# Optimization experiments

Hardware: AMD Instinct MI355X
Metric: run time of the kernel (lower is better)

The kernel has to match this reference:

```python
import jax, jax.numpy as jnp
import numpy as np

DECAY = 0.99
EPS = 1e-5
K = 1024  # num_embeddings
D = 64    # embedding_dim


def setup_inputs() -> dict:
    key = jax.random.key(0)
    k1, k2 = jax.random.split(key)
    inputs = jax.random.normal(k1, (64, 64, 32, 32), dtype=jnp.float32)
    weight = jax.random.uniform(k2, (K, D), minval=-1.0 / K, maxval=1.0 / K, dtype=jnp.float32)
    cluster_size = jnp.zeros((K,), dtype=jnp.float32)
    embed_avg = weight.copy()
    return {"inputs": inputs, "weight": weight, "cluster_size": cluster_size, "embed_avg": embed_avg}


def reference(inputs, weight, cluster_size, embed_avg):
    B, _, H, W = inputs.shape
    # faithful to torch: raw memory-order view(-1, D), no channel permute
    flat = inputs.reshape(-1, D)  # (N, D), N = B*H*W
    distances = (jnp.sum(flat * flat, axis=1, keepdims=True)
                 + jnp.sum(weight * weight, axis=1)
                 - 2.0 * flat @ weight.T)
    idx = jnp.argmin(distances, axis=1)  # (N,)
    quantized = weight[idx].reshape(inputs.shape)  # == onehot @ weight, reshaped

    # EMA codebook update (training path)
    counts = jax.ops.segment_sum(jnp.ones(flat.shape[0], dtype=jnp.float32), idx, num_segments=K)
    cs = DECAY * cluster_size + (1.0 - DECAY) * counts
    n = jnp.sum(cs)
    cs = (cs + EPS) / (n + K * EPS) * n
    dw = jax.ops.segment_sum(flat, idx, num_segments=K)  # == onehot^T @ flat
    new_embed_avg = DECAY * embed_avg + (1.0 - DECAY) * dw
    new_weight = new_embed_avg / cs[:, None]

    # straight-through estimator
    quantized_st = inputs + jax.lax.stop_gradient(quantized - inputs)
    indices = idx.reshape(B, H, W)
    return quantized_st, indices, new_weight, cs, new_embed_avg
```

## Files before the change

kernel.cpp:

```cpp
#include <hip/hip_runtime.h>

#define NROWS 65536
#define KC    1024
#define DD    64

#define QOFF  0
#define IOFF  4194304
#define WOFF  4259840
#define CSOFF 4325376
#define EAOFF 4326400

#define WS_CODESQ  0
#define WS_COUNTS  1056
#define WS_RCCNT   2080
#define WS_CURSOR  2096
#define WS_OFFS    3120
#define WS_CSFIN   4144
#define WS_DW      5168
#define WS_WSWZ    70704
#define WS_IDX     137264
#define WS_RCLIST  202800
#define WS_ROWLIST 268336
#define WS_PACKED  333872

#define MARGIN 5e-5f
#define DECIDED_BIT 0x10000

typedef _Float16 half8 __attribute__((ext_vector_type(8)));
typedef float    floatx4 __attribute__((ext_vector_type(4)));

struct F4 { float x, y, z, w; };
typedef const __attribute__((address_space(4))) F4    c4F4;
typedef const __attribute__((address_space(4))) float c4f;

__device__ __forceinline__ unsigned f2ord(float f) {
    unsigned u = __float_as_uint(f);
    return (u & 0x80000000u) ? ~u : (u | 0x80000000u);
}

__device__ __forceinline__ float med3f(float a, float b, float c) {
    float d;
    asm("v_med3_f32 %0, %1, %2, %3" : "=v"(d) : "v"(a), "v"(b), "v"(c));
    return d;
}

__device__ __forceinline__ float rowsq4(const float4* xv) {
    float4 re, ro;
    re.x = __fmul_rn(xv[0].x, xv[0].x); re.y = __fmul_rn(xv[0].y, xv[0].y);
    re.z = __fmul_rn(xv[0].z, xv[0].z); re.w = __fmul_rn(xv[0].w, xv[0].w);
    ro.x = __fmul_rn(xv[1].x, xv[1].x); ro.y = __fmul_rn(xv[1].y, xv[1].y);
    ro.z = __fmul_rn(xv[1].z, xv[1].z); ro.w = __fmul_rn(xv[1].w, xv[1].w);
#pragma unroll
    for (int i = 2; i < 16; i += 2) {
        re.x = __fadd_rn(re.x, __fmul_rn(xv[i].x, xv[i].x));
        re.y = __fadd_rn(re.y, __fmul_rn(xv[i].y, xv[i].y));
        re.z = __fadd_rn(re.z, __fmul_rn(xv[i].z, xv[i].z));
        re.w = __fadd_rn(re.w, __fmul_rn(xv[i].w, xv[i].w));
        ro.x = __fadd_rn(ro.x, __fmul_rn(xv[i + 1].x, xv[i + 1].x));
        ro.y = __fadd_rn(ro.y, __fmul_rn(xv[i + 1].y, xv[i + 1].y));
        ro.z = __fadd_rn(ro.z, __fmul_rn(xv[i + 1].z, xv[i + 1].z));
        ro.w = __fadd_rn(ro.w, __fmul_rn(xv[i + 1].w, xv[i + 1].w));
    }
    return __fadd_rn(__fadd_rn(__fadd_rn(re.x, re.y), __fadd_rn(re.z, re.w)),
                     __fadd_rn(__fadd_rn(ro.x, ro.y), __fadd_rn(ro.z, ro.w)));
}

__global__ void prep_kernel(const float* __restrict__ weight,
                            float* __restrict__ code_sq,
                            _Float16* __restrict__ wswz,
                            float* __restrict__ counts,
                            int* __restrict__ rccnt) {
    int c = blockIdx.x * blockDim.x + threadIdx.x;
    if (c >= KC) return;
    counts[c] = 0.0f;
    if (c == 0) rccnt[0] = 0;
    float4 wv4[16];
    const float4* pw = reinterpret_cast<const float4*>(weight + (size_t)c * DD);
#pragma unroll
    for (int i = 0; i < 16; ++i) wv4[i] = pw[i];
    code_sq[c] = rowsq4(wv4);
    float w64[64];
#pragma unroll
    for (int i = 0; i < 16; ++i) {
        w64[4 * i] = wv4[i].x; w64[4 * i + 1] = wv4[i].y;
        w64[4 * i + 2] = wv4[i].z; w64[4 * i + 3] = wv4[i].w;
    }
    const int t32 = c >> 5;
    const int s16 = (c >> 4) & 1;
    const int cl  = c & 15;
    const size_t base = (size_t)t32 * 4096 + s16 * 2048 + cl * 8;
#pragma unroll
    for (int q = 0; q < 8; ++q) {
        half8 h, l;
#pragma unroll
        for (int j = 0; j < 8; ++j) {
            float s = w64[q * 8 + j] * 1024.0f;
            _Float16 hh = (_Float16)s;
            h[j] = hh;
            l[j] = (_Float16)(s - (float)hh);
        }
        *reinterpret_cast<half8*>(wswz + base + q * 128)        = h;
        *reinterpret_cast<half8*>(wswz + base + 1024 + q * 128) = l;
    }
}

__global__ __launch_bounds__(256, 4) void vq_scan(
    const float* __restrict__ x_in, const float* __restrict__ weight,
    const float* __restrict__ code_sq, const _Float16* __restrict__ wswz,
    float* __restrict__ out, float* __restrict__ counts,
    int* __restrict__ idxbuf, int* __restrict__ rccnt, int* __restrict__ rclist,
    unsigned long long* __restrict__ packed) {

    __shared__ __align__(16) _Float16 lds_b[2][8192];
    __shared__ float lds_csq[KC];
    __shared__ float sm1[4][32], sm2[4][32];
    __shared__ int   si1[4][32];
    __shared__ int   idx_l[64];

    const int tid  = threadIdx.x;
    const int lane = tid & 63;
    const int w    = tid >> 6;
    const int wm   = w & 1;
    const int wsel = w >> 1;
    const int l15  = lane & 15;
    const int g    = lane >> 4;

    const int blockRow0 = blockIdx.x * 64;
    const int waveRow0  = blockRow0 + wm * 32;

    char* gsrc0 = const_cast<char*>(reinterpret_cast<const char*>(wswz));

#pragma unroll
    for (int j = 0; j < 4; ++j) {
        __builtin_amdgcn_global_load_lds(
            (__attribute__((address_space(1))) void*)(gsrc0 + tid * 16 + j * 4096),
            (__attribute__((address_space(3))) void*)((char*)lds_b[0] + tid * 16 + j * 4096),
            16, 0, 0);
    }

#pragma unroll
    for (int i = 0; i < 4; ++i) lds_csq[tid + i * 256] = code_sq[tid + i * 256];

    half8 ah[4], al[4];
#pragma unroll
    for (int t = 0; t < 2; ++t) {
#pragma unroll
        for (int kh = 0; kh < 2; ++kh) {
            const float4* p4 = reinterpret_cast<const float4*>(
                x_in + (size_t)(waveRow0 + t * 16 + l15) * DD + kh * 32 + g * 8);
            float4 v0 = p4[0], v1 = p4[1];
            float vals[8] = {v0.x, v0.y, v0.z, v0.w, v1.x, v1.y, v1.z, v1.w};
            half8 hh, ll;
#pragma unroll
            for (int j = 0; j < 8; ++j) {
                _Float16 h = (_Float16)vals[j];
                hh[j] = h;
                ll[j] = (_Float16)(vals[j] - (float)h);
            }
            ah[t * 2 + kh] = hh;
            al[t * 2 + kh] = ll;
        }
    }
    __syncthreads();

    float m1[2][4], m2[2][4];
    int   i1[2][4];
#pragma unroll
    for (int t = 0; t < 2; ++t)
#pragma unroll
        for (int r = 0; r < 4; ++r) { m1[t][r] = INFINITY; m2[t][r] = INFINITY; i1[t][r] = 0; }

    int cur = 0;
    for (int p = 0; p < 16; ++p) {
        if (p < 15) {
            char* src = gsrc0 + (size_t)(p + 1) * 16384;
            char* dst = (char*)lds_b[cur ^ 1];
#pragma unroll
            for (int j = 0; j < 4; ++j) {
                __builtin_amdgcn_global_load_lds(
                    (__attribute__((address_space(1))) void*)(src + tid * 16 + j * 4096),
                    (__attribute__((address_space(3))) void*)(dst + tid * 16 + j * 4096),
                    16, 0, 0);
            }
        }

#pragma unroll
        for (int half = 0; half < 2; ++half) {
            const _Float16* S = lds_b[cur] + half * 4096 + wsel * 2048;
            half8 bh0 = *reinterpret_cast<const half8*>(S + g * 128 + l15 * 8);
            half8 bh1 = *reinterpret_cast<const half8*>(S + 512 + g * 128 + l15 * 8);
            half8 bl0 = *reinterpret_cast<const half8*>(S + 1024 + g * 128 + l15 * 8);
            half8 bl1 = *reinterpret_cast<const half8*>(S + 1536 + g * 128 + l15 * 8);
            const int code = p * 64 + half * 32 + wsel * 16 + l15;
            const float csq = lds_csq[code];
#pragma unroll
            for (int t = 0; t < 2; ++t) {
                floatx4 c1 = {0.f, 0.f, 0.f, 0.f};
                floatx4 c2 = {0.f, 0.f, 0.f, 0.f};
                c1 = __builtin_amdgcn_mfma_f32_16x16x32_f16(al[t * 2 + 0], bh0, c1, 0, 0, 0);
                c2 = __builtin_amdgcn_mfma_f32_16x16x32_f16(al[t * 2 + 1], bh1, c2, 0, 0, 0);
                c1 = __builtin_amdgcn_mfma_f32_16x16x32_f16(ah[t * 2 + 0], bl0, c1, 0, 0, 0);
                c2 = __builtin_amdgcn_mfma_f32_16x16x32_f16(ah[t * 2 + 1], bl1, c2, 0, 0, 0);
                c1 = __builtin_amdgcn_mfma_f32_16x16x32_f16(ah[t * 2 + 0], bh0, c1, 0, 0, 0);
                c2 = __builtin_amdgcn_mfma_f32_16x16x32_f16(ah[t * 2 + 1], bh1, c2, 0, 0, 0);
#pragma unroll
                for (int r = 0; r < 4; ++r) {
                    float s = fmaf(c1[r] + c2[r], -0x1p-9f, csq);
                    float mo = m1[t][r];
                    m2[t][r] = med3f(s, mo, m2[t][r]);
                    i1[t][r] = (s < mo) ? code : i1[t][r];
                    m1[t][r] = fminf(mo, s);
                }
            }
        }

        __syncthreads();
        cur ^= 1;
    }

#pragma unroll
    for (int t = 0; t < 2; ++t)
#pragma unroll
        for (int r = 0; r < 4; ++r)
#pragma unroll
            for (int mk = 1; mk < 16; mk <<= 1) {
                float o1 = __shfl_xor(m1[t][r], mk);
                float o2 = __shfl_xor(m2[t][r], mk);
                int   oi = __shfl_xor(i1[t][r], mk);
                float n2 = fminf(fminf(m2[t][r], o2), fmaxf(m1[t][r], o1));
                bool sel = (o1 < m1[t][r]) || (o1 == m1[t][r] && oi < i1[t][r]);
                m1[t][r] = sel ? o1 : m1[t][r];
                i1[t][r] = sel ? oi : i1[t][r];
                m2[t][r] = n2;
            }

    if (l15 == 0) {
#pragma unroll
        for (int t = 0; t < 2; ++t)
#pragma unroll
            for (int r = 0; r < 4; ++r) {
                int rib = t * 16 + g * 4 + r;
                sm1[w][rib] = m1[t][r];
                sm2[w][rib] = m2[t][r];
                si1[w][rib] = i1[t][r];
            }
    }
    __syncthreads();

    if (tid < 64) {
        int pwm = tid >> 5;
        int rib = tid & 31;
        float bm1 = sm1[pwm][rib], bm2 = sm2[pwm][rib];
        int bi = si1[pwm][rib];
        {
            float v1 = sm1[pwm + 2][rib];
            float v2 = sm2[pwm + 2][rib];
            int   vi = si1[pwm + 2][rib];
            if (v1 < bm1 || (v1 == bm1 && vi < bi)) {
                bm2 = fminf(bm1, v2);
                bm1 = v1; bi = vi;
            } else {
                bm2 = fminf(bm2, v1);
            }
        }
        int grow = blockRow0 + tid;
        if (bm2 - bm1 >= MARGIN) {
            idxbuf[grow] = bi | DECIDED_BIT;
            out[IOFF + grow] = (float)bi;
            atomicAdd(&counts[bi], 1.0f);
            idx_l[tid] = bi;
        } else {
            packed[grow] = 0xFFFFFFFFFFFFFFFFull;
            int pos = atomicAdd(rccnt, 1);
            rclist[pos] = grow;
            idx_l[tid] = -1;
        }
    }
    __syncthreads();

    {
        const float4* xin4 = reinterpret_cast<const float4*>(x_in);
        const float4* w4g  = reinterpret_cast<const float4*>(weight);
        float4* q4 = reinterpret_cast<float4*>(out + QOFF);
        const size_t blk4 = (size_t)blockRow0 * 16;
#pragma unroll
        for (int j = 0; j < 4; ++j) {
            int f4i = tid + j * 256;
            int rl  = f4i >> 4;
            int d4  = f4i & 15;
            int idx = idx_l[rl];
            if (idx < 0) continue;
            float4 xq = xin4[blk4 + f4i];
            float4 wq = w4g[idx * 16 + d4];
            float4 qv;
            qv.x = __fadd_rn(xq.x, __fsub_rn(wq.x, xq.x));
            qv.y = __fadd_rn(xq.y, __fsub_rn(wq.y, xq.y));
            qv.z = __fadd_rn(xq.z, __fsub_rn(wq.z, xq.z));
            qv.w = __fadd_rn(xq.w, __fsub_rn(wq.w, xq.w));
            q4[blk4 + f4i] = qv;
        }
    }
}

__global__ __launch_bounds__(256, 4) void vq_recheck(
    const float* __restrict__ x_in, const float* __restrict__ weight,
    const float* __restrict__ code_sq,
    unsigned long long* __restrict__ packed,
    const int* __restrict__ rccnt, const int* __restrict__ rclist) {

    const int nrc = rccnt[0];
    const int nitems = ((nrc + 63) >> 6) * 16;

    const int tid  = threadIdx.x;
    const int lane = tid & 63;
    const int wvu  = __builtin_amdgcn_readfirstlane(tid >> 6);

    for (int item = blockIdx.x; item < nitems; item += gridDim.x) {
        const int rb     = (item >> 4) * 64;
        const int cchunk = item & 15;
        const bool valid = (rb + lane) < nrc;
        const int  grow  = rclist[valid ? rb + lane : rb];

        float4 xv[16];
        const float4* px = reinterpret_cast<const float4*>(x_in + (size_t)grow * DD);
#pragma unroll
        for (int i = 0; i < 16; ++i) xv[i] = px[i];
        const float rs = rowsq4(xv);

        const int k0 = cchunk * 64 + wvu * 16;
        unsigned long long wa = (unsigned long long)(weight + (size_t)k0 * DD);
        unsigned long long ca = (unsigned long long)(code_sq + k0);
        unsigned wal = __builtin_amdgcn_readfirstlane((unsigned)wa);
        unsigned wah = __builtin_amdgcn_readfirstlane((unsigned)(wa >> 32));
        unsigned cal = __builtin_amdgcn_readfirstlane((unsigned)ca);
        unsigned cah = __builtin_amdgcn_readfirstlane((unsigned)(ca >> 32));
        c4F4* wb4 = (c4F4*)(((unsigned long long)wah << 32) | wal);
        c4f*  cb  = (c4f*)(((unsigned long long)cah << 32) | cal);

        float best = INFINITY;
        int bidx = 0x7fffffff;

#pragma unroll 2
        for (int k = 0; k < 16; ++k) {
            float a0 = 0.f, a1 = 0.f, a2 = 0.f, a3 = 0.f;
#pragma unroll
            for (int i = 0; i < 16; ++i) {
                F4 w4;
                w4.x = wb4[k * 16 + i].x;
                w4.y = wb4[k * 16 + i].y;
                w4.z = wb4[k * 16 + i].z;
                w4.w = wb4[k * 16 + i].w;
                a0 += xv[i].x * w4.x;
                a1 += xv[i].y * w4.y;
                a2 += xv[i].z * w4.z;
                a3 += xv[i].w * w4.w;
            }
            float dot = (a0 + a1) + (a2 + a3);
            float csq = cb[k];
            float dst = __fsub_rn(__fadd_rn(rs, csq), __fmul_rn(2.0f, dot));
            int kg = k0 + k;
            if (dst < best) { best = dst; bidx = kg; }
        }

        if (valid) {
            unsigned long long p =
                ((unsigned long long)f2ord(best) << 32) | (unsigned)bidx;
            atomicMin(&packed[grow], p);
        }
    }
}

__global__ void rc_offsets_cs(const unsigned long long* __restrict__ packed,
                              const int* __restrict__ rccnt,
                              const int* __restrict__ rclist,
                              const float* __restrict__ cluster_size,
                              float* __restrict__ out, int* __restrict__ idxbuf,
                              float* __restrict__ counts,
                              int* __restrict__ offs, int* __restrict__ cursor,
                              float* __restrict__ cs_fin) {
    __shared__ int   hist[1024];
    __shared__ int   sc[1024];
    __shared__ float sb[1024];
    int k = threadIdx.x;
    hist[k] = 0;
    __syncthreads();
    const int nrc = rccnt[0];
    for (int i = k; i < nrc; i += 1024) {
        int grow = rclist[i];
        int bidx = (int)(packed[grow] & 0xFFFFFFFFull);
        out[IOFF + grow] = (float)bidx;
        idxbuf[grow] = bidx;
        atomicAdd(&hist[bidx], 1);
    }
    __syncthreads();
    int c = (int)counts[k] + hist[k];
    counts[k] = (float)c;
    float ce = 0.99f * cluster_size[k] + 0.01f * (float)c;
    sc[k] = c;
    sb[k] = ce;
    __syncthreads();
    for (int off = 1; off < 1024; off <<= 1) {
        int v = (k >= off) ? sc[k - off] : 0;
        __syncthreads();
        sc[k] += v;
        __syncthreads();
    }
    offs[k] = sc[k] - c;
    cursor[k] = 0;
    for (int off = 512; off > 0; off >>= 1) {
        if (k < off) sb[k] += sb[k + off];
        __syncthreads();
    }
    float n = sb[0];
    float v = ((ce + 1e-5f) / (n + 0.01024f)) * n;
    out[CSOFF + k] = v;
    cs_fin[k] = v;
}

__global__ void scatter_kernel(const int* __restrict__ idxbuf,
                               const int* __restrict__ offs,
                               int* __restrict__ cursor,
                               int* __restrict__ rowlist) {
    int r = blockIdx.x * blockDim.x + threadIdx.x;
    if (r >= NROWS) return;
    int v = idxbuf[r];
    int k = v & 1023;
    int pos = atomicAdd(&cursor[k], 1);
    rowlist[offs[k] + pos] = r | ((v & DECIDED_BIT) ? 0 : 0x80000000);
}

__global__ __launch_bounds__(512) void dw_q_kernel(
    const float* __restrict__ x_in,
    const float* __restrict__ weight,
    const float* __restrict__ counts,
    const int* __restrict__ offs,
    const int* __restrict__ rowlist,
    const float* __restrict__ embed_avg,
    const float* __restrict__ cs_fin,
    float* __restrict__ out, float* __restrict__ dw) {
    __shared__ float wsh[64];
    __shared__ float part[8][64];

    const int k    = blockIdx.x;
    const int tid  = threadIdx.x;
    const int lane = tid & 63;
    const int wv   = tid >> 6;

    if (tid < 64) wsh[tid] = weight[(size_t)k * DD + tid];
    __syncthreads();

    const int cnt  = (int)counts[k];
    const int base = offs[k];
    const float wk = wsh[lane];

    float acc = 0.f;
    int i = wv;
    for (; i + 24 < cnt; i += 32) {
        int e0 = rowlist[base + i];
        int e1 = rowlist[base + i + 8];
        int e2 = rowlist[base + i + 16];
        int e3 = rowlist[base + i + 24];
        int r0 = e0 & 0x7fffffff;
        int r1 = e1 & 0x7fffffff;
        int r2 = e2 & 0x7fffffff;
        int r3 = e3 & 0x7fffffff;
        float x0 = x_in[(size_t)r0 * DD + lane];
        float x1 = x_in[(size_t)r1 * DD + lane];
        float x2 = x_in[(size_t)r2 * DD + lane];
        float x3 = x_in[(size_t)r3 * DD + lane];
        if (e0 < 0) out[QOFF + (size_t)r0 * DD + lane] = __fadd_rn(x0, __fsub_rn(wk, x0));
        if (e1 < 0) out[QOFF + (size_t)r1 * DD + lane] = __fadd_rn(x1, __fsub_rn(wk, x1));
        if (e2 < 0) out[QOFF + (size_t)r2 * DD + lane] = __fadd_rn(x2, __fsub_rn(wk, x2));
        if (e3 < 0) out[QOFF + (size_t)r3 * DD + lane] = __fadd_rn(x3, __fsub_rn(wk, x3));
        acc = __fadd_rn(acc, x0);
        acc = __fadd_rn(acc, x1);
        acc = __fadd_rn(acc, x2);
        acc = __fadd_rn(acc, x3);
    }
    for (; i < cnt; i += 8) {
        int e = rowlist[base + i];
        int r = e & 0x7fffffff;
        float xq = x_in[(size_t)r * DD + lane];
        if (e < 0) out[QOFF + (size_t)r * DD + lane] = __fadd_rn(xq, __fsub_rn(wk, xq));
        acc = __fadd_rn(acc, xq);
    }
    part[wv][lane] = acc;
    __syncthreads();
    if (tid < 64) {
        float s01 = __fadd_rn(part[0][tid], part[1][tid]);
        float s23 = __fadd_rn(part[2][tid], part[3][tid]);
        float s45 = __fadd_rn(part[4][tid], part[5][tid]);
        float s67 = __fadd_rn(part[6][tid], part[7][tid]);
        float s = __fadd_rn(__fadd_rn(s01, s23), __fadd_rn(s45, s67));
        int e = k * DD + tid;
        dw[e] = s;
        float na = 0.99f * embed_avg[e] + 0.01f * s;
        out[EAOFF + e] = na;
        out[WOFF + e] = na / cs_fin[k];
    }
}

extern "C" void kernel_launch(void* const* d_in, const int* in_sizes, int n_in,
                              void* d_out, int out_size, void* d_ws, size_t ws_size,
                              hipStream_t stream) {
    (void)in_sizes; (void)n_in; (void)out_size; (void)ws_size;
    const float* x       = (const float*)d_in[0];
    const float* weight  = (const float*)d_in[1];
    const float* cluster = (const float*)d_in[2];
    const float* eavg    = (const float*)d_in[3];
    float* out = (float*)d_out;
    float* wsf = (float*)d_ws;

    float*    code_sq = wsf + WS_CODESQ;
    float*    counts  = wsf + WS_COUNTS;
    int*      rccnt   = (int*)(wsf + WS_RCCNT);
    int*      cursor  = (int*)(wsf + WS_CURSOR);
    int*      offs    = (int*)(wsf + WS_OFFS);
    float*    cs_fin  = wsf + WS_CSFIN;
    float*    dwbuf   = wsf + WS_DW;
    _Float16* wswz    = (_Float16*)(wsf + WS_WSWZ);
    int*      idxbuf  = (int*)(wsf + WS_IDX);
    int*      rclist  = (int*)(wsf + WS_RCLIST);
    int*      rowlist = (int*)(wsf + WS_ROWLIST);
    unsigned long long* packed = (unsigned long long*)(wsf + WS_PACKED);

    hipLaunchKernelGGL(prep_kernel, dim3(16), dim3(64), 0, stream,
                       weight, code_sq, wswz, counts, rccnt);
    hipLaunchKernelGGL(vq_scan, dim3(1024), dim3(256), 0, stream,
                       x, weight, code_sq, wswz, out, counts, idxbuf, rccnt,
                       rclist, packed);
    hipLaunchKernelGGL(vq_recheck, dim3(2048), dim3(256), 0, stream,
                       x, weight, code_sq, packed, rccnt, rclist);
    hipLaunchKernelGGL(rc_offsets_cs, dim3(1), dim3(1024), 0, stream,
                       packed, rccnt, rclist, cluster, out, idxbuf, counts,
                       offs, cursor, cs_fin);
    hipLaunchKernelGGL(scatter_kernel, dim3(256), dim3(256), 0, stream,
                       idxbuf, offs, cursor, rowlist);
    hipLaunchKernelGGL(dw_q_kernel, dim3(1024), dim3(512), 0, stream,
                       x, weight, counts, offs, rowlist, eavg, cs_fin, out, dwbuf);
}
```

Baseline: 115.8 us.

## Give each wave a private double-buffered codebook tile and drop block barriers

```diff
diff --git a/kernel.cpp b/kernel.cpp
--- a/kernel.cpp
+++ b/kernel.cpp
@@ -111,7 +111,7 @@
     int* __restrict__ idxbuf, int* __restrict__ rccnt, int* __restrict__ rclist,
     unsigned long long* __restrict__ packed) {
 
-    __shared__ __align__(16) _Float16 lds_b[2][8192];
+    __shared__ __align__(16) _Float16 lds_b[4][2][2048];
     __shared__ float lds_csq[KC];
     __shared__ float sm1[4][32], sm2[4][32];
     __shared__ int   si1[4][32];
@@ -128,15 +128,22 @@
     const int blockRow0 = blockIdx.x * 64;
     const int waveRow0  = blockRow0 + wm * 32;
 
-    char* gsrc0 = const_cast<char*>(reinterpret_cast<const char*>(wswz));
-
-#pragma unroll
-    for (int j = 0; j < 4; ++j) {
-        __builtin_amdgcn_global_load_lds(
-            (__attribute__((address_space(1))) void*)(gsrc0 + tid * 16 + j * 4096),
-            (__attribute__((address_space(3))) void*)((char*)lds_b[0] + tid * 16 + j * 4096),
-            16, 0, 0);
-    }
+    const char* gsrc0 = reinterpret_cast<const char*>(wswz);
+    const size_t wbase = (size_t)wsel * 4096;
+
+#define DMA_SUBTILE(i_, b_) do {                                              \
+        const char* s_ = gsrc0 + wbase + (size_t)(i_) * 8192;                 \
+        char* d_ = (char*)lds_b[w][b_];                                       \
+        _Pragma("unroll")                                                     \
+        for (int j_ = 0; j_ < 4; ++j_) {                                      \
+            __builtin_amdgcn_global_load_lds(                                 \
+                (__attribute__((address_space(1))) void*)(s_ + lane * 16 + j_ * 1024), \
+                (__attribute__((address_space(3))) void*)(d_ + lane * 16 + j_ * 1024), \
+                16, 0, 0);                                                    \
+        }                                                                     \
+    } while (0)
+
+    DMA_SUBTILE(0, 0);
 
 #pragma unroll
     for (int i = 0; i < 4; ++i) lds_csq[tid + i * 256] = code_sq[tid + i * 256];
@@ -170,53 +177,47 @@
 #pragma unroll
         for (int r = 0; r < 4; ++r) { m1[t][r] = INFINITY; m2[t][r] = INFINITY; i1[t][r] = 0; }
 
-    int cur = 0;
-    for (int p = 0; p < 16; ++p) {
-        if (p < 15) {
-            char* src = gsrc0 + (size_t)(p + 1) * 16384;
-            char* dst = (char*)lds_b[cur ^ 1];
-#pragma unroll
-            for (int j = 0; j < 4; ++j) {
-                __builtin_amdgcn_global_load_lds(
-                    (__attribute__((address_space(1))) void*)(src + tid * 16 + j * 4096),
-                    (__attribute__((address_space(3))) void*)(dst + tid * 16 + j * 4096),
-                    16, 0, 0);
-            }
-        }
-
-#pragma unroll
-        for (int half = 0; half < 2; ++half) {
-            const _Float16* S = lds_b[cur] + half * 4096 + wsel * 2048;
-            half8 bh0 = *reinterpret_cast<const half8*>(S + g * 128 + l15 * 8);
-            half8 bh1 = *reinterpret_cast<const half8*>(S + 512 + g * 128 + l15 * 8);
-            half8 bl0 = *reinterpret_cast<const half8*>(S + 1024 + g * 128 + l15 * 8);
-            half8 bl1 = *reinterpret_cast<const half8*>(S + 1536 + g * 128 + l15 * 8);
-            const int code = p * 64 + half * 32 + wsel * 16 + l15;
-            const float csq = lds_csq[code];
-#pragma unroll
-            for (int t = 0; t < 2; ++t) {
-                floatx4 c1 = {0.f, 0.f, 0.f, 0.f};
-                floatx4 c2 = {0.f, 0.f, 0.f, 0.f};
-                c1 = __builtin_amdgcn_mfma_f32_16x16x32_f16(al[t * 2 + 0], bh0, c1, 0, 0, 0);
-                c2 = __builtin_amdgcn_mfma_f32_16x16x32_f16(al[t * 2 + 1], bh1, c2, 0, 0, 0);
-                c1 = __builtin_amdgcn_mfma_f32_16x16x32_f16(ah[t * 2 + 0], bl0, c1, 0, 0, 0);
-                c2 = __builtin_amdgcn_mfma_f32_16x16x32_f16(ah[t * 2 + 1], bl1, c2, 0, 0, 0);
-                c1 = __builtin_amdgcn_mfma_f32_16x16x32_f16(ah[t * 2 + 0], bh0, c1, 0, 0, 0);
-                c2 = __builtin_amdgcn_mfma_f32_16x16x32_f16(ah[t * 2 + 1], bh1, c2, 0, 0, 0);
-#pragma unroll
-                for (int r = 0; r < 4; ++r) {
-                    float s = fmaf(c1[r] + c2[r], -0x1p-9f, csq);
-                    float mo = m1[t][r];
-                    m2[t][r] = med3f(s, mo, m2[t][r]);
-                    i1[t][r] = (s < mo) ? code : i1[t][r];
-                    m1[t][r] = fminf(mo, s);
-                }
-            }
-        }
-
-        __syncthreads();
-        cur ^= 1;
-    }
+#define COMPUTE_SUBTILE(i_, b_) do {                                          \
+        const _Float16* S = lds_b[w][b_];                                     \
+        half8 bh0 = *reinterpret_cast<const half8*>(S + g * 128 + l15 * 8);   \
+        half8 bh1 = *reinterpret_cast<const half8*>(S + 512 + g * 128 + l15 * 8); \
+        half8 bl0 = *reinterpret_cast<const half8*>(S + 1024 + g * 128 + l15 * 8); \
+        half8 bl1 = *reinterpret_cast<const half8*>(S + 1536 + g * 128 + l15 * 8); \
+        const int code = (i_) * 32 + wsel * 16 + l15;                         \
+        const float csq = lds_csq[code];                                      \
+        _Pragma("unroll")                                                     \
+        for (int t = 0; t < 2; ++t) {                                         \
+            floatx4 c1 = {0.f, 0.f, 0.f, 0.f};                                \
+            floatx4 c2 = {0.f, 0.f, 0.f, 0.f};                                \
+            c1 = __builtin_amdgcn_mfma_f32_16x16x32_f16(al[t * 2 + 0], bh0, c1, 0, 0, 0); \
+            c2 = __builtin_amdgcn_mfma_f32_16x16x32_f16(al[t * 2 + 1], bh1, c2, 0, 0, 0); \
+            c1 = __builtin_amdgcn_mfma_f32_16x16x32_f16(ah[t * 2 + 0], bl0, c1, 0, 0, 0); \
+            c2 = __builtin_amdgcn_mfma_f32_16x16x32_f16(ah[t * 2 + 1], bl1, c2, 0, 0, 0); \
+            c1 = __builtin_amdgcn_mfma_f32_16x16x32_f16(ah[t * 2 + 0], bh0, c1, 0, 0, 0); \
+            c2 = __builtin_amdgcn_mfma_f32_16x16x32_f16(ah[t * 2 + 1], bh1, c2, 0, 0, 0); \
+            _Pragma("unroll")                                                 \
+            for (int r = 0; r < 4; ++r) {                                     \
+                float s = fmaf(c1[r] + c2[r], -0x1p-9f, csq);                 \
+                float mo = m1[t][r];                                          \
+                m2[t][r] = med3f(s, mo, m2[t][r]);                            \
+                i1[t][r] = (s < mo) ? code : i1[t][r];                        \
+                m1[t][r] = fminf(mo, s);                                      \
+            }                                                                 \
+        }                                                                     \
+    } while (0)
+
+    for (int i = 0; i < 31; ++i) {
+        DMA_SUBTILE(i + 1, (i + 1) & 1);
+        asm volatile("s_waitcnt vmcnt(4)" ::: "memory");
+        __builtin_amdgcn_sched_barrier(0);
+        COMPUTE_SUBTILE(i, i & 1);
+    }
+    asm volatile("s_waitcnt vmcnt(0)" ::: "memory");
+    __builtin_amdgcn_sched_barrier(0);
+    COMPUTE_SUBTILE(31, 1);
+
+#undef DMA_SUBTILE
+#undef COMPUTE_SUBTILE
 
 #pragma unroll
     for (int t = 0; t < 2; ++t)
```

After: 124.0 us. +7.1%, slower.
